# Performance work log

Hardware: AMD Instinct MI355X
Metric: run time of the kernel (lower is better)

## Reference

```python
import jax, jax.numpy as jnp
import numpy as np

B, S, D, H = 2, 2048, 1024, 16
DK = D // H

def setup_inputs() -> dict:
    key = jax.random.key(0)
    ks = jax.random.split(key, 9)
    def lin(k, fan_in):
        bound = 1.0 / np.sqrt(fan_in)
        kw, kb = jax.random.split(k)
        w = jax.random.uniform(kw, (D, D), jnp.float32, -bound, bound)
        b = jax.random.uniform(kb, (D,), jnp.float32, -bound, bound)
        return w, b
    Wq_w, Wq_b = lin(ks[0], D)
    Wk_w, Wk_b = lin(ks[1], D)
    Wv_w, Wv_b = lin(ks[2], D)
    Wo_w, Wo_b = lin(ks[3], D)
    x = jax.random.normal(ks[4], (B, S, D), jnp.float32)
    mask = jnp.ones((B, 1, 1, S), jnp.int32)
    return {"x": x, "mask": mask,
            "Wq_w": Wq_w, "Wq_b": Wq_b, "Wk_w": Wk_w, "Wk_b": Wk_b,
            "Wv_w": Wv_w, "Wv_b": Wv_b, "Wo_w": Wo_w, "Wo_b": Wo_b}

def reference(x, mask, Wq_w, Wq_b, Wk_w, Wk_b, Wv_w, Wv_b, Wo_w, Wo_b):
    b, s, d = x.shape
    def split_heads(t):  # [B,S,D] -> [B,H,S,DK]
        return t.reshape(b, s, H, DK).transpose(0, 2, 1, 3)
    Q = split_heads(x @ Wq_w.T + Wq_b)
    K = split_heads(x @ Wk_w.T + Wk_b)
    V = split_heads(x @ Wv_w.T + Wv_b)
    scale = 1.0 / jnp.sqrt(jnp.float32(DK))
    scores = jnp.einsum('bhqd,bhkd->bhqk', Q, K) * scale  # [B,H,S,S]
    scores = jnp.where(mask == 0, jnp.float32(-1e9), scores)
    attn = jax.nn.softmax(scores, axis=-1)
    context = jnp.einsum('bhqk,bhkd->bhqd', attn, V)  # [B,H,S,DK]
    context = context.transpose(0, 2, 1, 3).reshape(b, s, d)
    return context @ Wo_w.T + Wo_b
```

## Files before the change

kernel.cpp:

```cpp
#include <hip/hip_runtime.h>
#include <hip/hip_bf16.h>


#define DEV __device__ __forceinline__

typedef __bf16 bf16_t;
typedef __bf16 bf16x4 __attribute__((ext_vector_type(4)));
typedef __bf16 bf16x8 __attribute__((ext_vector_type(8)));
typedef float f32x4 __attribute__((ext_vector_type(4)));

constexpr int Ss = 2048, Dd = 1024, Hh = 16, DKk = 64;

DEV void gload_lds16(const void* g, void* l) {
  __builtin_amdgcn_global_load_lds(
      (__attribute__((address_space(1))) void*)(g),
      (__attribute__((address_space(3))) void*)(l), 16, 0, 0);
}

DEV bf16_t f2b(float v) { return (bf16_t)v; }

DEV void cvt16_core(const float* src, bf16_t* dst) {
  const float4* s4 = (const float4*)src;
  float4 a = s4[0], b = s4[1], c = s4[2], d = s4[3];
  bf16x8 lo = {f2b(a.x), f2b(a.y), f2b(a.z), f2b(a.w), f2b(b.x), f2b(b.y), f2b(b.z), f2b(b.w)};
  bf16x8 hi = {f2b(c.x), f2b(c.y), f2b(c.z), f2b(c.w), f2b(d.x), f2b(d.y), f2b(d.z), f2b(d.w)};
  *(bf16x8*)dst = lo;
  *(bf16x8*)(dst + 8) = hi;
}

__global__ __launch_bounds__(256) void cvt16(const float* __restrict__ x,
                                             bf16_t* __restrict__ xb) {
  size_t i = ((size_t)blockIdx.x * 256 + threadIdx.x) * 16;
  cvt16_core(x + i, xb + i);
}

__global__ __launch_bounds__(256) void cvt_all(
    const float* __restrict__ x,
    const float* __restrict__ wq, const float* __restrict__ wk,
    const float* __restrict__ wv, const float* __restrict__ wo,
    bf16_t* __restrict__ xb, bf16_t* __restrict__ Wb) {
  size_t i = ((size_t)blockIdx.x * 256 + threadIdx.x) * 16;
  const size_t XN = (size_t)4 << 20;
  if (i < XN) {
    cvt16_core(x + i, xb + i);
  } else {
    size_t j = i - XN;
    int z = (int)(j >> 20);
    size_t o = j & (((size_t)1 << 20) - 1);
    const float* s = (z == 0) ? wq : ((z == 1) ? wk : ((z == 2) ? wv : wo));
    cvt16_core(s + o, Wb + j);
  }
}

template <bool WB16>
__global__ __launch_bounds__(256) void gemm_qkv(
    const bf16_t* __restrict__ A,
    const float* __restrict__ W0, const float* __restrict__ W1, const float* __restrict__ W2,
    const bf16_t* __restrict__ Wb,
    const float* __restrict__ b0, const float* __restrict__ b1, const float* __restrict__ b2,
    bf16_t* __restrict__ o0, bf16_t* __restrict__ o1, bf16_t* __restrict__ o2) {
  const int z = blockIdx.z;
  const float* Wf = (z == 0) ? W0 : ((z == 1) ? W1 : W2);
  const bf16_t* Wbf = Wb + (size_t)z * (1u << 20);
  const float* bias = (z == 0) ? b0 : ((z == 1) ? b1 : b2);
  bf16_t* out = (z == 0) ? o0 : ((z == 1) ? o1 : o2);

  __shared__ __align__(16) bf16_t As[128 * 32];
  __shared__ __align__(16) bf16_t Ws[128 * 32];

  const int tid = threadIdx.x;
  const int lane = tid & 63, w = tid >> 6;
  const int quad = lane >> 4, c = lane & 15;
  const int wm = w >> 1, wn = w & 1;
  const int m0 = blockIdx.y * 128, n0 = blockIdx.x * 128;
  const int trow = tid >> 1, tcol = (tid & 1) * 16;
  const int srow = lane >> 2, scol = (lane & 3) * 8;

  const f32x4 vzero = {0.f, 0.f, 0.f, 0.f};
  f32x4 acc[4][4];
  for (int i = 0; i < 4; i++)
    for (int j = 0; j < 4; j++) acc[i][j] = vzero;

  for (int k0 = 0; k0 < 1024; k0 += 32) {
    for (int r = 0; r < 2; r++) {
      int row = r * 64 + w * 16;
      gload_lds16(&A[(size_t)(m0 + row + srow) * 1024 + k0 + scol], &As[row * 32]);
      if (WB16)
        gload_lds16(&Wbf[(size_t)(n0 + row + srow) * 1024 + k0 + scol], &Ws[row * 32]);
    }
    if (!WB16)
      cvt16_core(&Wf[(size_t)(n0 + trow) * 1024 + k0 + tcol], &Ws[trow * 32 + tcol]);
    __syncthreads();

    bf16x8 af[4], bfr[4];
    for (int i = 0; i < 4; i++)
      af[i] = *(const bf16x8*)&As[(wm * 64 + i * 16 + c) * 32 + quad * 8];
    for (int j = 0; j < 4; j++)
      bfr[j] = *(const bf16x8*)&Ws[(wn * 64 + j * 16 + c) * 32 + quad * 8];
    for (int i = 0; i < 4; i++)
      for (int j = 0; j < 4; j++)
        acc[i][j] = __builtin_amdgcn_mfma_f32_16x16x32_bf16(af[i], bfr[j], acc[i][j], 0, 0, 0);
    __syncthreads();
  }

  for (int j = 0; j < 4; j++) {
    int n = n0 + wn * 64 + j * 16 + c;
    float bv = bias[n];
    for (int i = 0; i < 4; i++) {
      int mbase = m0 + wm * 64 + i * 16 + quad * 4;
      int b_ = mbase >> 11, s_ = mbase & 2047;
      int h_ = n >> 6, dk_ = n & 63;
      if (z < 2) {
        for (int r = 0; r < 4; r++)
          out[((size_t)(b_ * Hh + h_) * Ss + (s_ + r)) * DKk + dk_] =
              f2b(acc[i][j][r] + bv);
      } else {
        bf16x4 pk;
        for (int r = 0; r < 4; r++) pk[r] = f2b(acc[i][j][r] + bv);
        *(bf16x4*)&out[((size_t)(b_ * Hh + h_) * DKk + dk_) * Ss + s_] = pk;
      }
    }
  }
}

__global__ __launch_bounds__(256) void attn_fwd(
    const bf16_t* __restrict__ Q, const bf16_t* __restrict__ K,
    const bf16_t* __restrict__ Vt, const int* __restrict__ mask,
    bf16_t* __restrict__ ctx) {
  __shared__ __align__(16) bf16_t Ks[2][64 * 64];
  __shared__ __align__(16) bf16_t Vts[2][64 * 64];
  __shared__ __align__(16) bf16_t Ps[4][32 * 64];

  const int tid = threadIdx.x, lane = tid & 63, w = tid >> 6;
  const int quad = lane >> 4, c = lane & 15;
  const int c7 = c & 7;
  const int bh = blockIdx.y, b_ = bh >> 4, h_ = bh & 15;
  const int q0 = blockIdx.x * 128 + w * 32;
  const size_t head = (size_t)bh * Ss * DKk;
  const int* maskb = mask + b_ * Ss;

  const int sr = lane >> 3;
  const int gc = (lane & 7) ^ sr;

  {
    for (int r = 0; r < 2; r++) {
      int row = r * 32 + w * 8;
      gload_lds16(&K[head + (size_t)(row + sr) * 64 + gc * 8], &Ks[0][row * 64]);
      gload_lds16(&Vt[head + (size_t)(row + sr) * Ss + gc * 8], &Vts[0][row * 64]);
    }
  }

  bf16x8 qf[2][2];
  for (int mi = 0; mi < 2; mi++)
    for (int ks = 0; ks < 2; ks++)
      qf[mi][ks] = *(const bf16x8*)&Q[head + (size_t)(q0 + mi * 16 + c) * DKk + ks * 32 + quad * 8];

  int mk[4];
  for (int ni = 0; ni < 4; ni++) mk[ni] = maskb[ni * 16 + c];

  const bf16_t oneb = f2b(1.0f);
  const bf16x8 ones = {oneb, oneb, oneb, oneb, oneb, oneb, oneb, oneb};

  const f32x4 vzero = {0.f, 0.f, 0.f, 0.f};
  f32x4 o[2][4];
  for (int mi = 0; mi < 2; mi++)
    for (int j = 0; j < 4; j++) o[mi][j] = vzero;
  f32x4 ol[2] = {vzero, vzero};

  constexpr int NT = Ss / 64;
  for (int kt = 0; kt < NT; kt++) {
    const int cur = kt & 1;
    __syncthreads();

    if (kt + 1 < NT) {
      int nxt = cur ^ 1;
      for (int r = 0; r < 2; r++) {
        int row = r * 32 + w * 8;
        gload_lds16(&K[head + (size_t)((kt + 1) * 64 + row + sr) * 64 + gc * 8],
                    &Ks[nxt][row * 64]);
        gload_lds16(&Vt[head + (size_t)(row + sr) * Ss + (kt + 1) * 64 + gc * 8],
                    &Vts[nxt][row * 64]);
      }
    }
    int mkn[4];
    if (kt + 1 < NT)
      for (int ni = 0; ni < 4; ni++) mkn[ni] = maskb[(kt + 1) * 64 + ni * 16 + c];

    f32x4 sc[2][4];
    for (int mi = 0; mi < 2; mi++)
      for (int ni = 0; ni < 4; ni++) sc[mi][ni] = vzero;
    for (int ks = 0; ks < 2; ks++) {
      int pc = ((ks * 4 + quad) ^ c7) * 8;
      for (int ni = 0; ni < 4; ni++) {
        bf16x8 kf = *(const bf16x8*)&Ks[cur][(ni * 16 + c) * 64 + pc];
        sc[0][ni] = __builtin_amdgcn_mfma_f32_16x16x32_bf16(qf[0][ks], kf, sc[0][ni], 0, 0, 0);
        sc[1][ni] = __builtin_amdgcn_mfma_f32_16x16x32_bf16(qf[1][ks], kf, sc[1][ni], 0, 0, 0);
      }
    }

    for (int ni = 0; ni < 4; ni++) {
      for (int mi = 0; mi < 2; mi++)
        for (int r = 0; r < 4; r++) {
          float p = __expf(sc[mi][ni][r] * 0.125f);
          sc[mi][ni][r] = mk[ni] ? p : 0.f;
        }
    }

    for (int mi = 0; mi < 2; mi++)
      for (int ni = 0; ni < 4; ni++)
        for (int r = 0; r < 4; r++) {
          int ql = mi * 16 + quad * 4 + r;
          int chunk = (ni * 2 + (c >> 3)) ^ (ql & 7);
          Ps[w][ql * 64 + chunk * 8 + c7] = f2b(sc[mi][ni][r]);
        }

    for (int ks = 0; ks < 2; ks++) {
      int pc = ((ks * 4 + quad) ^ c7) * 8;
      bf16x8 pf0 = *(const bf16x8*)&Ps[w][(c)*64 + pc];
      bf16x8 pf1 = *(const bf16x8*)&Ps[w][(16 + c) * 64 + pc];
      for (int j = 0; j < 4; j++) {
        bf16x8 vf = *(const bf16x8*)&Vts[cur][(j * 16 + c) * 64 + pc];
        o[0][j] = __builtin_amdgcn_mfma_f32_16x16x32_bf16(pf0, vf, o[0][j], 0, 0, 0);
        o[1][j] = __builtin_amdgcn_mfma_f32_16x16x32_bf16(pf1, vf, o[1][j], 0, 0, 0);
      }
      ol[0] = __builtin_amdgcn_mfma_f32_16x16x32_bf16(pf0, ones, ol[0], 0, 0, 0);
      ol[1] = __builtin_amdgcn_mfma_f32_16x16x32_bf16(pf1, ones, ol[1], 0, 0, 0);
    }

    for (int ni = 0; ni < 4; ni++) mk[ni] = mkn[ni];
  }

  for (int mi = 0; mi < 2; mi++) {
    float inv[4];
    for (int r = 0; r < 4; r++) inv[r] = 1.0f / ol[mi][r];
    for (int j = 0; j < 4; j++)
      for (int r = 0; r < 4; r++) {
        int s_ = q0 + mi * 16 + quad * 4 + r;
        ctx[((size_t)(b_ * Ss + s_)) * Dd + h_ * 64 + j * 16 + c] =
            f2b(o[mi][j][r] * inv[r]);
      }
  }
}

template <bool WB16>
__global__ __launch_bounds__(256) void gemm_out(
    const bf16_t* __restrict__ A, const float* __restrict__ Wf,
    const bf16_t* __restrict__ Wb, const float* __restrict__ bias,
    float* __restrict__ out) {
  __shared__ __align__(16) bf16_t As[64 * 32];
  __shared__ __align__(16) bf16_t Ws[128 * 32];

  const int tid = threadIdx.x;
  const int lane = tid & 63, w = tid >> 6;
  const int quad = lane >> 4, c = lane & 15;
  const int wm = w >> 1, wn = w & 1;
  const int m0 = blockIdx.y * 64, n0 = blockIdx.x * 128;
  const int trow = tid >> 1, tcol = (tid & 1) * 16;
  const int srow = lane >> 2, scol = (lane & 3) * 8;

  const f32x4 vzero = {0.f, 0.f, 0.f, 0.f};
  f32x4 acc[2][4];
  for (int i = 0; i < 2; i++)
    for (int j = 0; j < 4; j++) acc[i][j] = vzero;

  for (int k0 = 0; k0 < 1024; k0 += 32) {
    gload_lds16(&A[(size_t)(m0 + w * 16 + srow) * 1024 + k0 + scol], &As[(w * 16) * 32]);
    if (WB16) {
      for (int r = 0; r < 2; r++) {
        int row = r * 64 + w * 16;
        gload_lds16(&Wb[(size_t)(n0 + row + srow) * 1024 + k0 + scol], &Ws[row * 32]);
      }
    } else {
      cvt16_core(&Wf[(size_t)(n0 + trow) * 1024 + k0 + tcol], &Ws[trow * 32 + tcol]);
    }
    __syncthreads();

    bf16x8 af[2], bfr[4];
    for (int i = 0; i < 2; i++)
      af[i] = *(const bf16x8*)&As[(wm * 32 + i * 16 + c) * 32 + quad * 8];
    for (int j = 0; j < 4; j++)
      bfr[j] = *(const bf16x8*)&Ws[(wn * 64 + j * 16 + c) * 32 + quad * 8];
    for (int i = 0; i < 2; i++)
      for (int j = 0; j < 4; j++)
        acc[i][j] = __builtin_amdgcn_mfma_f32_16x16x32_bf16(af[i], bfr[j], acc[i][j], 0, 0, 0);
    __syncthreads();
  }

  for (int j = 0; j < 4; j++) {
    int n = n0 + wn * 64 + j * 16 + c;
    float bv = bias[n];
    for (int i = 0; i < 2; i++) {
      int mbase = m0 + wm * 32 + i * 16 + quad * 4;
      for (int r = 0; r < 4; r++)
        out[(size_t)(mbase + r) * 1024 + n] = acc[i][j][r] + bv;
    }
  }
}

extern "C" void kernel_launch(void* const* d_in, const int* in_sizes, int n_in,
                              void* d_out, int out_size, void* d_ws, size_t ws_size,
                              hipStream_t stream) {
  const float* x  = (const float*)d_in[0];
  const int* mask = (const int*)d_in[1];
  const float* Wq = (const float*)d_in[2];
  const float* bq = (const float*)d_in[3];
  const float* Wk = (const float*)d_in[4];
  const float* bk = (const float*)d_in[5];
  const float* Wv = (const float*)d_in[6];
  const float* bv = (const float*)d_in[7];
  const float* Wo = (const float*)d_in[8];
  const float* bo = (const float*)d_in[9];
  float* out = (float*)d_out;

  bf16_t* ws = (bf16_t*)d_ws;
  const size_t QKV_ELEMS = (size_t)2 * Hh * Ss * DKk;
  bf16_t* xb  = ws;
  bf16_t* Qb  = ws + QKV_ELEMS;
  bf16_t* Kb  = ws + 2 * QKV_ELEMS;
  bf16_t* Vt  = ws + 3 * QKV_ELEMS;
  bf16_t* Wb  = ws + 4 * QKV_ELEMS;
  bf16_t* ctx = xb;

  const bool wb16 = ws_size >= (size_t)40 * 1024 * 1024;

  if (wb16) {
    cvt_all<<<dim3(2048), 256, 0, stream>>>(x, Wq, Wk, Wv, Wo, xb, Wb);
    gemm_qkv<true><<<dim3(8, 32, 3), 256, 0, stream>>>(
        xb, Wq, Wk, Wv, Wb, bq, bk, bv, Qb, Kb, Vt);
  } else {
    cvt16<<<dim3(1024), 256, 0, stream>>>(x, xb);
    gemm_qkv<false><<<dim3(8, 32, 3), 256, 0, stream>>>(
        xb, Wq, Wk, Wv, ws , bq, bk, bv, Qb, Kb, Vt);
  }
  attn_fwd<<<dim3(Ss / 128, 2 * Hh), 256, 0, stream>>>(Qb, Kb, Vt, mask, ctx);
  if (wb16)
    gemm_out<true><<<dim3(8, 64), 256, 0, stream>>>(ctx, Wo, Wb + 3 * (1u << 20), bo, out);
  else
    gemm_out<false><<<dim3(8, 64), 256, 0, stream>>>(ctx, Wo, ws , bo, out);
}
```

Measured before the change: 217.6 us.

## Rewrite attention with 32x32 MFMA, in-register P transpose, and XCD-aware tile mapping

Switches the attention inner loop from 16x16x32 to 32x32x16 MFMA and computes S^T = K·Q^T, so the probability tile can be packed to bf16 with v_cvt_pk_bf16_f32 and rearranged across lanes with v_permlane32_swap. This removes the per-wave LDS round trip for P. The softmax scale is folded into the Q projection epilogue. The mask is loaded once per tile with a ballot, and a fast path skips per-element selects when the mask is all ones. It also remaps blocks so that heads are grouped per XCD for L2 locality and raises wave priority around the MFMA sections. The cost is more complex lane-layout logic and a different output store pattern.

Result: faster. 199.7 us (-8.2%).

```diff
diff --git a/kernel.cpp b/kernel.cpp
--- a/kernel.cpp
+++ b/kernel.cpp
@@ -8,6 +8,8 @@
 typedef __bf16 bf16x4 __attribute__((ext_vector_type(4)));
 typedef __bf16 bf16x8 __attribute__((ext_vector_type(8)));
 typedef float f32x4 __attribute__((ext_vector_type(4)));
+typedef float f32x16 __attribute__((ext_vector_type(16)));
+typedef unsigned int u32;
 
 constexpr int Ss = 2048, Dd = 1024, Hh = 16, DKk = 64;
 
@@ -18,6 +20,16 @@
 }
 
 DEV bf16_t f2b(float v) { return (bf16_t)v; }
+
+DEV u32 cvtpk(float lo, float hi) {
+  u32 r;
+  asm("v_cvt_pk_bf16_f32 %0, %1, %2" : "=v"(r) : "v"(lo), "v"(hi));
+  return r;
+}
+
+DEV void swap32(u32& a, u32& b) {
+  asm("v_permlane32_swap_b32 %0, %1" : "+v"(a), "+v"(b));
+}
 
 DEV void cvt16_core(const float* src, bf16_t* dst) {
   const float4* s4 = (const float4*)src;
@@ -64,6 +76,7 @@
   const bf16_t* Wbf = Wb + (size_t)z * (1u << 20);
   const float* bias = (z == 0) ? b0 : ((z == 1) ? b1 : b2);
   bf16_t* out = (z == 0) ? o0 : ((z == 1) ? o1 : o2);
+  const float scl = (z == 0) ? 0.125f : 1.0f;
 
   __shared__ __align__(16) bf16_t As[128 * 32];
   __shared__ __align__(16) bf16_t Ws[128 * 32];
@@ -113,7 +126,7 @@
       if (z < 2) {
         for (int r = 0; r < 4; r++)
           out[((size_t)(b_ * Hh + h_) * Ss + (s_ + r)) * DKk + dk_] =
-              f2b(acc[i][j][r] + bv);
+              f2b((acc[i][j][r] + bv) * scl);
       } else {
         bf16x4 pk;
         for (int r = 0; r < 4; r++) pk[r] = f2b(acc[i][j][r] + bv);
@@ -129,48 +142,47 @@
     bf16_t* __restrict__ ctx) {
   __shared__ __align__(16) bf16_t Ks[2][64 * 64];
   __shared__ __align__(16) bf16_t Vts[2][64 * 64];
-  __shared__ __align__(16) bf16_t Ps[4][32 * 64];
 
   const int tid = threadIdx.x, lane = tid & 63, w = tid >> 6;
-  const int quad = lane >> 4, c = lane & 15;
-  const int c7 = c & 7;
-  const int bh = blockIdx.y, b_ = bh >> 4, h_ = bh & 15;
-  const int q0 = blockIdx.x * 128 + w * 32;
+  const int m = lane & 31, hi = lane >> 5;
+
+  const int fid = (int)(blockIdx.y * gridDim.x + blockIdx.x);
+  const int xcd = fid & 7, j_ = fid >> 3;
+  const int bh = xcd * 4 + (j_ >> 4);
+  const int qblk = j_ & 15;
+
+  const int b_ = bh >> 4, h_ = bh & 15;
+  const int q0 = qblk * 128 + w * 32;
   const size_t head = (size_t)bh * Ss * DKk;
   const int* maskb = mask + b_ * Ss;
 
   const int sr = lane >> 3;
   const int gc = (lane & 7) ^ sr;
 
-  {
-    for (int r = 0; r < 2; r++) {
-      int row = r * 32 + w * 8;
-      gload_lds16(&K[head + (size_t)(row + sr) * 64 + gc * 8], &Ks[0][row * 64]);
-      gload_lds16(&Vt[head + (size_t)(row + sr) * Ss + gc * 8], &Vts[0][row * 64]);
-    }
-  }
-
-  bf16x8 qf[2][2];
-  for (int mi = 0; mi < 2; mi++)
-    for (int ks = 0; ks < 2; ks++)
-      qf[mi][ks] = *(const bf16x8*)&Q[head + (size_t)(q0 + mi * 16 + c) * DKk + ks * 32 + quad * 8];
-
-  int mk[4];
-  for (int ni = 0; ni < 4; ni++) mk[ni] = maskb[ni * 16 + c];
+  for (int r = 0; r < 2; r++) {
+    int row = r * 32 + w * 8;
+    gload_lds16(&K[head + (size_t)(row + sr) * 64 + gc * 8], &Ks[0][row * 64]);
+    gload_lds16(&Vt[head + (size_t)(row + sr) * Ss + gc * 8], &Vts[0][row * 64]);
+  }
+
+  bf16x8 qf[4];
+#pragma unroll
+  for (int ks = 0; ks < 4; ks++)
+    qf[ks] = *(const bf16x8*)&Q[head + (size_t)(q0 + m) * 64 + ks * 16 + hi * 8];
 
   const bf16_t oneb = f2b(1.0f);
   const bf16x8 ones = {oneb, oneb, oneb, oneb, oneb, oneb, oneb, oneb};
 
-  const f32x4 vzero = {0.f, 0.f, 0.f, 0.f};
-  f32x4 o[2][4];
-  for (int mi = 0; mi < 2; mi++)
-    for (int j = 0; j < 4; j++) o[mi][j] = vzero;
-  f32x4 ol[2] = {vzero, vzero};
+  f32x16 o0, o1, ol;
+#pragma unroll
+  for (int i = 0; i < 16; i++) { o0[i] = 0.f; o1[i] = 0.f; ol[i] = 0.f; }
 
   constexpr int NT = Ss / 64;
   for (int kt = 0; kt < NT; kt++) {
     const int cur = kt & 1;
     __syncthreads();
+
+    int mv = maskb[kt * 64 + lane];
 
     if (kt + 1 < NT) {
       int nxt = cur ^ 1;
@@ -182,63 +194,73 @@
                     &Vts[nxt][row * 64]);
       }
     }
-    int mkn[4];
-    if (kt + 1 < NT)
-      for (int ni = 0; ni < 4; ni++) mkn[ni] = maskb[(kt + 1) * 64 + ni * 16 + c];
-
-    f32x4 sc[2][4];
-    for (int mi = 0; mi < 2; mi++)
-      for (int ni = 0; ni < 4; ni++) sc[mi][ni] = vzero;
-    for (int ks = 0; ks < 2; ks++) {
-      int pc = ((ks * 4 + quad) ^ c7) * 8;
-      for (int ni = 0; ni < 4; ni++) {
-        bf16x8 kf = *(const bf16x8*)&Ks[cur][(ni * 16 + c) * 64 + pc];
-        sc[0][ni] = __builtin_amdgcn_mfma_f32_16x16x32_bf16(qf[0][ks], kf, sc[0][ni], 0, 0, 0);
-        sc[1][ni] = __builtin_amdgcn_mfma_f32_16x16x32_bf16(qf[1][ks], kf, sc[1][ni], 0, 0, 0);
+
+    f32x16 sc[2];
+#pragma unroll
+    for (int i = 0; i < 16; i++) { sc[0][i] = 0.f; sc[1][i] = 0.f; }
+
+    __builtin_amdgcn_s_setprio(1);
+#pragma unroll
+    for (int ks = 0; ks < 4; ks++) {
+      const int pc = ((ks * 2 + hi) ^ (m & 7)) * 8;
+      bf16x8 k0 = *(const bf16x8*)&Ks[cur][m * 64 + pc];
+      bf16x8 k1 = *(const bf16x8*)&Ks[cur][(32 + m) * 64 + pc];
+      sc[0] = __builtin_amdgcn_mfma_f32_32x32x16_bf16(k0, qf[ks], sc[0], 0, 0, 0);
+      sc[1] = __builtin_amdgcn_mfma_f32_32x32x16_bf16(k1, qf[ks], sc[1], 0, 0, 0);
+    }
+    __builtin_amdgcn_s_setprio(0);
+
+    unsigned long long bits = __ballot(mv != 0);
+    if (bits == ~0ull) {
+#pragma unroll
+      for (int nt = 0; nt < 2; nt++)
+#pragma unroll
+        for (int i = 0; i < 16; i++) sc[nt][i] = __expf(sc[nt][i]);
+    } else {
+#pragma unroll
+      for (int nt = 0; nt < 2; nt++) {
+        u32 wb = (u32)(bits >> (nt * 32));
+        u32 wsh = hi ? (wb >> 4) : wb;
+#pragma unroll
+        for (int i = 0; i < 16; i++) {
+          int bitpos = 8 * (i >> 2) + (i & 3);
+          sc[nt][i] = ((wsh >> bitpos) & 1u) ? __expf(sc[nt][i]) : 0.f;
+        }
       }
     }
 
-    for (int ni = 0; ni < 4; ni++) {
-      for (int mi = 0; mi < 2; mi++)
-        for (int r = 0; r < 4; r++) {
-          float p = __expf(sc[mi][ni][r] * 0.125f);
-          sc[mi][ni][r] = mk[ni] ? p : 0.f;
-        }
-    }
-
-    for (int mi = 0; mi < 2; mi++)
-      for (int ni = 0; ni < 4; ni++)
-        for (int r = 0; r < 4; r++) {
-          int ql = mi * 16 + quad * 4 + r;
-          int chunk = (ni * 2 + (c >> 3)) ^ (ql & 7);
-          Ps[w][ql * 64 + chunk * 8 + c7] = f2b(sc[mi][ni][r]);
-        }
-
-    for (int ks = 0; ks < 2; ks++) {
-      int pc = ((ks * 4 + quad) ^ c7) * 8;
-      bf16x8 pf0 = *(const bf16x8*)&Ps[w][(c)*64 + pc];
-      bf16x8 pf1 = *(const bf16x8*)&Ps[w][(16 + c) * 64 + pc];
-      for (int j = 0; j < 4; j++) {
-        bf16x8 vf = *(const bf16x8*)&Vts[cur][(j * 16 + c) * 64 + pc];
-        o[0][j] = __builtin_amdgcn_mfma_f32_16x16x32_bf16(pf0, vf, o[0][j], 0, 0, 0);
-        o[1][j] = __builtin_amdgcn_mfma_f32_16x16x32_bf16(pf1, vf, o[1][j], 0, 0, 0);
-      }
-      ol[0] = __builtin_amdgcn_mfma_f32_16x16x32_bf16(pf0, ones, ol[0], 0, 0, 0);
-      ol[1] = __builtin_amdgcn_mfma_f32_16x16x32_bf16(pf1, ones, ol[1], 0, 0, 0);
-    }
-
-    for (int ni = 0; ni < 4; ni++) mk[ni] = mkn[ni];
-  }
-
-  for (int mi = 0; mi < 2; mi++) {
-    float inv[4];
-    for (int r = 0; r < 4; r++) inv[r] = 1.0f / ol[mi][r];
-    for (int j = 0; j < 4; j++)
-      for (int r = 0; r < 4; r++) {
-        int s_ = q0 + mi * 16 + quad * 4 + r;
-        ctx[((size_t)(b_ * Ss + s_)) * Dd + h_ * 64 + j * 16 + c] =
-            f2b(o[mi][j][r] * inv[r]);
-      }
+    __builtin_amdgcn_s_setprio(1);
+#pragma unroll
+    for (int t = 0; t < 4; t++) {
+      const int nt = t >> 1, gA = 2 * (t & 1), gB = gA + 1;
+      u32 a0 = cvtpk(sc[nt][4 * gA + 0], sc[nt][4 * gA + 1]);
+      u32 a1 = cvtpk(sc[nt][4 * gA + 2], sc[nt][4 * gA + 3]);
+      u32 b0 = cvtpk(sc[nt][4 * gB + 0], sc[nt][4 * gB + 1]);
+      u32 b1 = cvtpk(sc[nt][4 * gB + 2], sc[nt][4 * gB + 3]);
+      swap32(a0, b0);
+      swap32(a1, b1);
+      int4 wv = {(int)a0, (int)a1, (int)b0, (int)b1};
+      bf16x8 pa = __builtin_bit_cast(bf16x8, wv);
+
+      ol = __builtin_amdgcn_mfma_f32_32x32x16_bf16(pa, ones, ol, 0, 0, 0);
+      const int pc = ((t * 2 + hi) ^ (m & 7)) * 8;
+      bf16x8 v0 = *(const bf16x8*)&Vts[cur][m * 64 + pc];
+      bf16x8 v1 = *(const bf16x8*)&Vts[cur][(32 + m) * 64 + pc];
+      o0 = __builtin_amdgcn_mfma_f32_32x32x16_bf16(pa, v0, o0, 0, 0, 0);
+      o1 = __builtin_amdgcn_mfma_f32_32x32x16_bf16(pa, v1, o1, 0, 0, 0);
+    }
+    __builtin_amdgcn_s_setprio(0);
+  }
+
+  f32x16 inv;
+#pragma unroll
+  for (int r = 0; r < 16; r++) inv[r] = 1.0f / ol[r];
+#pragma unroll
+  for (int r = 0; r < 16; r++) {
+    int s_ = q0 + (r & 3) + 8 * (r >> 2) + 4 * hi;
+    size_t base = ((size_t)(b_ * Ss + s_)) * Dd + h_ * 64;
+    ctx[base + m] = f2b(o0[r] * inv[r]);
+    ctx[base + 32 + m] = f2b(o1[r] * inv[r]);
   }
 }
 
```
